# Kernel tuning notes

Hardware: AMD Instinct MI355X
Metric: run time of the kernel (lower is better)

Reference implementation:

```python
import jax, jax.numpy as jnp
import numpy as np

T, B, D, H, O = 512, 256, 512, 256, 256
MLP_DIMS = [(D, 100), (100, 100), (100, 100), (100, 50), (50, H)]


def _linear_init(key, fan_in, fan_out):
    kw, kb = jax.random.split(key)
    lim = 1.0 / np.sqrt(fan_in)
    w = jax.random.uniform(kw, (fan_out, fan_in), minval=-lim, maxval=lim, dtype=jnp.float32)
    b = jax.random.uniform(kb, (fan_out,), minval=-lim, maxval=lim, dtype=jnp.float32)
    return w, b


def setup_inputs() -> dict:
    key = jax.random.key(0)
    ks = jax.random.split(key, 8)
    inp = {"x": jax.random.normal(ks[0], (T, B, D), dtype=jnp.float32)}
    for i, (fi, fo) in enumerate(MLP_DIMS):
        w, b = _linear_init(ks[1 + i], fi, fo)
        inp[f"wm{i + 1}"] = w
        inp[f"bm{i + 1}"] = b
    inp["wx"], inp["bx"] = _linear_init(ks[6], D, H)
    inp["wo"], inp["bo"] = _linear_init(ks[7], H, O)
    return inp


def reference(x, wm1, bm1, wm2, bm2, wm3, bm3, wm4, bm4, wm5, bm5, wx, bx, wo, bo):
    def step(h, xt):
        # xt: [B, D], h: [B, H]
        lx = xt @ wx.T + bx                      # linearX
        a = jax.nn.relu(xt @ wm1.T + bm1)        # layerMLP chain
        a = jax.nn.relu(a @ wm2.T + bm2)
        a = jax.nn.relu(a @ wm3.T + bm3)
        a = jax.nn.relu(a @ wm4.T + bm4)
        fx = jax.nn.sigmoid(a @ wm5.T + bm5)
        gate = fx * jax.nn.sigmoid(lx)
        h_new = jax.nn.relu(jnp.roll(h, 1, axis=-1) + gate)
        return h_new, None

    h0 = jnp.zeros((x.shape[1], wx.shape[0]), dtype=x.dtype)
    hidden, _ = jax.lax.scan(step, h0, x)
    output = hidden @ wo.T + bo                  # h2o
    return output, hidden
```

## Files before the change

kernel.cpp:

```cpp
#include <hip/hip_runtime.h>

typedef __attribute__((ext_vector_type(8))) short short8;
typedef __attribute__((ext_vector_type(4))) float f32x4;

#define OFF_WX 0
#define OFF_W1 131072
#define OFF_W2 188416
#define OFF_W3 202752
#define OFF_W4 217088
#define OFF_W5 225280
#define W_TOTAL 241664

#define TR 32

static __device__ __forceinline__ unsigned short f2bf(float f) {
    unsigned int u = __builtin_bit_cast(unsigned int, f);
    unsigned int r = (u + 0x7fffu + ((u >> 16) & 1u)) >> 16;
    return (unsigned short)r;
}
static __device__ __forceinline__ float bf2f(unsigned short h) {
    unsigned int u = ((unsigned int)h) << 16;
    return __builtin_bit_cast(float, u);
}
static __device__ __forceinline__ float sigmoidf(float z) {
    return 1.f / (1.f + __expf(-z));
}

__global__ __launch_bounds__(256) void prep_kernel(
    const float* __restrict__ wx, const float* __restrict__ wm1,
    const float* __restrict__ wm2, const float* __restrict__ wm3,
    const float* __restrict__ wm4, const float* __restrict__ wm5,
    unsigned short* __restrict__ wb, float* __restrict__ hid)
{
    const int stride = gridDim.x * blockDim.x;
    for (int idx = blockIdx.x * blockDim.x + threadIdx.x; idx < W_TOTAL; idx += stride) {
        float v;
        if (idx < OFF_W1) {
            v = wx[idx];
        } else if (idx < OFF_W2) {
            int j = idx - OFF_W1; int n = j >> 9, k = j & 511;
            v = (n < 100) ? wm1[n * 512 + k] : 0.f;
        } else if (idx < OFF_W3) {
            int j = idx - OFF_W2; int n = j >> 7, k = j & 127;
            v = (n < 100 && k < 100) ? wm2[n * 100 + k] : 0.f;
        } else if (idx < OFF_W4) {
            int j = idx - OFF_W3; int n = j >> 7, k = j & 127;
            v = (n < 100 && k < 100) ? wm3[n * 100 + k] : 0.f;
        } else if (idx < OFF_W5) {
            int j = idx - OFF_W4; int n = j >> 7, k = j & 127;
            v = (n < 50 && k < 100) ? wm4[n * 100 + k] : 0.f;
        } else {
            int j = idx - OFF_W5; int n = j >> 6, k = j & 63;
            v = (k < 50) ? wm5[n * 50 + k] : 0.f;
        }
        wb[idx] = f2bf(v);
    }
    for (int idx = blockIdx.x * blockDim.x + threadIdx.x; idx < 65536; idx += stride)
        hid[idx] = 0.f;
}

template<int KPAD, int NT, int APITCH, int MT, typename Epi>
static __device__ __forceinline__ void stage(const unsigned short* As,
                                             const unsigned short* __restrict__ Wg,
                                             int wave, int lane, Epi&& epi)
{
    constexpr int NI = (NT + 3) >> 2;
    f32x4 acc[NI][MT];
#pragma unroll
    for (int i = 0; i < NI; i++)
#pragma unroll
        for (int mt = 0; mt < MT; mt++)
            acc[i][mt] = {0.f, 0.f, 0.f, 0.f};

    const int kp  = (lane >> 4) << 3;
    const int l15 = lane & 15;

#pragma unroll 4
    for (int k0 = 0; k0 < KPAD; k0 += 32) {
        short8 af[MT];
#pragma unroll
        for (int mt = 0; mt < MT; mt++)
            af[mt] = *(const short8*)(As + (mt * 16 + l15) * APITCH + k0 + kp);
#pragma unroll
        for (int i = 0; i < NI; i++) {
            const int nt = wave + (i << 2);
            if (nt < NT) {
                short8 bf = *(const short8*)(Wg + (nt * 16 + l15) * KPAD + k0 + kp);
#pragma unroll
                for (int mt = 0; mt < MT; mt++)
                    acc[i][mt] = __builtin_amdgcn_mfma_f32_16x16x32_bf16(
                        af[mt], bf, acc[i][mt], 0, 0, 0);
            }
        }
    }
#pragma unroll
    for (int i = 0; i < NI; i++) {
        const int nt = wave + (i << 2);
        if (nt < NT) {
#pragma unroll
            for (int mt = 0; mt < MT; mt++)
                epi(i, nt, mt, acc[i][mt]);
        }
    }
}

__global__ __launch_bounds__(256, 3) void srnn_main(
    const float* __restrict__ x,
    const float* __restrict__ b1, const float* __restrict__ b2,
    const float* __restrict__ b3, const float* __restrict__ b4,
    const float* __restrict__ b5, const float* __restrict__ bx,
    const unsigned short* __restrict__ wb, float* __restrict__ hid)
{
    __shared__ __align__(16) unsigned short Xs[TR * 520];
    __shared__ __align__(16) unsigned short ABuf[2 * TR * 136];
    unsigned short* A1 = ABuf;
    unsigned short* A2 = ABuf + TR * 136;
    unsigned short* Gs = ABuf;

    const int tid  = threadIdx.x;
    const int wave = tid >> 6, lane = tid & 63;
    const int blk  = blockIdx.x;
    const int b    = blk >> 4;
    const int t0   = (blk & 15) << 5;
    const int l15  = lane & 15;
    const int rbase = (lane >> 4) << 2;

    for (int f = tid; f < TR * 128; f += 256) {
        int m = f >> 7, c4 = f & 127;
        const float4* src = (const float4*)(x + ((size_t)(t0 + m) * 256 + b) * 512);
        float4 v = src[c4];
        unsigned int p0 = (unsigned int)f2bf(v.x) | ((unsigned int)f2bf(v.y) << 16);
        unsigned int p1 = (unsigned int)f2bf(v.z) | ((unsigned int)f2bf(v.w) << 16);
        *(uint2*)&Xs[m * 520 + (c4 << 2)] = make_uint2(p0, p1);
    }
    for (int i = tid; i < (2 * TR * 136) / 4; i += 256)
        ((uint2*)ABuf)[i] = make_uint2(0u, 0u);
    __syncthreads();

    stage<512, 7, 520, 2>(Xs, wb + OFF_W1, wave, lane, [&](int, int nt, int mt, f32x4 v) {
        int c = nt * 16 + l15, r = mt * 16 + rbase;
        float bb = (c < 100) ? b1[c] : 0.f;
#pragma unroll
        for (int q = 0; q < 4; q++) {
            float val = (c < 100) ? fmaxf(v[q] + bb, 0.f) : 0.f;
            A1[(r + q) * 136 + c] = f2bf(val);
        }
    });
    __syncthreads();

    stage<128, 7, 136, 2>(A1, wb + OFF_W2, wave, lane, [&](int, int nt, int mt, f32x4 v) {
        int c = nt * 16 + l15, r = mt * 16 + rbase;
        float bb = (c < 100) ? b2[c] : 0.f;
#pragma unroll
        for (int q = 0; q < 4; q++) {
            float val = (c < 100) ? fmaxf(v[q] + bb, 0.f) : 0.f;
            A2[(r + q) * 136 + c] = f2bf(val);
        }
    });
    __syncthreads();

    stage<128, 7, 136, 2>(A2, wb + OFF_W3, wave, lane, [&](int, int nt, int mt, f32x4 v) {
        int c = nt * 16 + l15, r = mt * 16 + rbase;
        float bb = (c < 100) ? b3[c] : 0.f;
#pragma unroll
        for (int q = 0; q < 4; q++) {
            float val = (c < 100) ? fmaxf(v[q] + bb, 0.f) : 0.f;
            A1[(r + q) * 136 + c] = f2bf(val);
        }
    });
    __syncthreads();

    stage<128, 4, 136, 2>(A1, wb + OFF_W4, wave, lane, [&](int, int nt, int mt, f32x4 v) {
        int c = nt * 16 + l15, r = mt * 16 + rbase;
        float bb = (c < 50) ? b4[c] : 0.f;
#pragma unroll
        for (int q = 0; q < 4; q++) {
            float val = (c < 50) ? fmaxf(v[q] + bb, 0.f) : 0.f;
            A2[(r + q) * 136 + c] = f2bf(val);
        }
    });
    __syncthreads();

    f32x4 fxv[4][2];
    stage<64, 16, 136, 2>(A2, wb + OFF_W5, wave, lane, [&](int i, int nt, int mt, f32x4 v) {
        float bb = b5[nt * 16 + l15];
#pragma unroll
        for (int q = 0; q < 4; q++)
            fxv[i][mt][q] = sigmoidf(v[q] + bb);
    });
    __syncthreads();

    stage<512, 16, 520, 2>(Xs, wb + OFF_WX, wave, lane, [&](int i, int nt, int mt, f32x4 v) {
        int c = nt * 16 + l15, r = mt * 16 + rbase;
        float bb = bx[c];
#pragma unroll
        for (int q = 0; q < 4; q++) {
            float g = sigmoidf(v[q] + bb) * fxv[i][mt][q];
            Gs[(r + q) * 264 + c] = f2bf(g);
        }
    });
    __syncthreads();

    {
        const int j = tid;
        const int base = (j + t0 + 1) & 255;
        float ph = 0.f;
#pragma unroll 8
        for (int m = 0; m < TR; m++)
            ph += bf2f(Gs[m * 264 + ((base + m) & 255)]);
        atomicAdd(hid + b * 256 + j, ph);
    }
}

__global__ __launch_bounds__(256) void out_kernel(
    const float* __restrict__ hid, const float* __restrict__ wo,
    const float* __restrict__ bo, float* __restrict__ out)
{
    __shared__ __align__(16) float hrow[256];
    const int b = blockIdx.x, o = threadIdx.x;
    float h = hid[b * 256 + o];
    hrow[o] = h;
    out[65536 + b * 256 + o] = h;
    __syncthreads();
    const float4* wrow = (const float4*)(wo + o * 256);
    float s = bo[o];
#pragma unroll 8
    for (int k4 = 0; k4 < 64; k4++) {
        float4 w = wrow[k4];
        float4 hh = *(const float4*)&hrow[k4 * 4];
        s += hh.x * w.x + hh.y * w.y + hh.z * w.z + hh.w * w.w;
    }
    out[b * 256 + o] = s;
}

extern "C" void kernel_launch(void* const* d_in, const int* in_sizes, int n_in,
                              void* d_out, int out_size, void* d_ws, size_t ws_size,
                              hipStream_t stream)
{
    (void)in_sizes; (void)n_in; (void)out_size; (void)ws_size;
    const float* x   = (const float*)d_in[0];
    const float* wm1 = (const float*)d_in[1];
    const float* bm1 = (const float*)d_in[2];
    const float* wm2 = (const float*)d_in[3];
    const float* bm2 = (const float*)d_in[4];
    const float* wm3 = (const float*)d_in[5];
    const float* bm3 = (const float*)d_in[6];
    const float* wm4 = (const float*)d_in[7];
    const float* bm4 = (const float*)d_in[8];
    const float* wm5 = (const float*)d_in[9];
    const float* bm5 = (const float*)d_in[10];
    const float* wx  = (const float*)d_in[11];
    const float* bx  = (const float*)d_in[12];
    const float* wo  = (const float*)d_in[13];
    const float* bo  = (const float*)d_in[14];
    float* out = (float*)d_out;

    unsigned short* wb = (unsigned short*)d_ws;
    float* hid = (float*)((char*)d_ws + (size_t)W_TOTAL * 2);

    prep_kernel<<<512, 256, 0, stream>>>(wx, wm1, wm2, wm3, wm4, wm5, wb, hid);
    srnn_main<<<4096, 256, 0, stream>>>(x, bm1, bm2, bm3, bm4, bm5, bx, wb, hid);
    out_kernel<<<256, 256, 0, stream>>>(hid, wo, bo, out);
}
```

Baseline: 640.4 us.

## Fuse W1 and Wx GEMMs, swizzle LDS layouts, raise occupancy

The first MLP layer and the linearX projection now run in one K-loop that shares the same X fragment loads, instead of two separate passes over Xs. Padded LDS row pitches are replaced by XOR-swizzled 128/512-element rows, and buffers are aliased to shrink shared memory. This allows raising launch bounds to 4 blocks per CU. The x tile load is also restructured to issue 16 float4 loads per thread before converting, and the ABuf zero-fill is dropped. Fusing keeps more accumulators live, which raises register pressure at the higher occupancy target.

```diff
diff --git a/kernel.cpp b/kernel.cpp
--- a/kernel.cpp
+++ b/kernel.cpp
@@ -5,12 +5,11 @@
 
 #define OFF_WX 0
 #define OFF_W1 131072
-#define OFF_W2 188416
-#define OFF_W3 202752
-#define OFF_W4 217088
-#define OFF_W5 225280
-#define W_TOTAL 241664
-
+#define OFF_W2 196608
+#define OFF_W3 212992
+#define OFF_W4 229376
+#define OFF_W5 237568
+#define W_TOTAL 253952
 #define TR 32
 
 static __device__ __forceinline__ unsigned short f2bf(float f) {
@@ -24,6 +23,9 @@
 }
 static __device__ __forceinline__ float sigmoidf(float z) {
     return 1.f / (1.f + __expf(-z));
+}
+static __device__ __forceinline__ void stA(unsigned short* dst, int r, int c, float v) {
+    dst[(r << 7) + (((c >> 3) ^ (r & 7)) << 3) + (c & 7)] = f2bf(v);
 }
 
 __global__ __launch_bounds__(256) void prep_kernel(
@@ -59,63 +61,53 @@
         hid[idx] = 0.f;
 }
 
-template<int KPAD, int NT, int APITCH, int MT, typename Epi>
-static __device__ __forceinline__ void stage(const unsigned short* As,
-                                             const unsigned short* __restrict__ Wg,
-                                             int wave, int lane, Epi&& epi)
-{
-    constexpr int NI = (NT + 3) >> 2;
-    f32x4 acc[NI][MT];
-#pragma unroll
-    for (int i = 0; i < NI; i++)
-#pragma unroll
-        for (int mt = 0; mt < MT; mt++)
-            acc[i][mt] = {0.f, 0.f, 0.f, 0.f};
-
+template<int KLOOP, int NI, typename Epi>
+static __device__ __forceinline__ void stageS(const unsigned short* As,
+                                              const unsigned short* __restrict__ Wg,
+                                              int wave, int lane, Epi&& epi)
+{
+    f32x4 acc[NI][2];
+#pragma unroll
+    for (int i = 0; i < NI; i++) { acc[i][0] = {0,0,0,0}; acc[i][1] = {0,0,0,0}; }
     const int kp  = (lane >> 4) << 3;
     const int l15 = lane & 15;
-
-#pragma unroll 4
-    for (int k0 = 0; k0 < KPAD; k0 += 32) {
-        short8 af[MT];
-#pragma unroll
-        for (int mt = 0; mt < MT; mt++)
-            af[mt] = *(const short8*)(As + (mt * 16 + l15) * APITCH + k0 + kp);
+#pragma unroll
+    for (int k0 = 0; k0 < KLOOP; k0 += 32) {
+        const int kb = (k0 >> 3) + (lane >> 4);
+        short8 af[2];
+#pragma unroll
+        for (int mt = 0; mt < 2; mt++) {
+            const int rm = mt * 16 + l15;
+            af[mt] = *(const short8*)(As + (rm << 7) + ((kb ^ (rm & 7)) << 3));
+        }
 #pragma unroll
         for (int i = 0; i < NI; i++) {
             const int nt = wave + (i << 2);
-            if (nt < NT) {
-                short8 bf = *(const short8*)(Wg + (nt * 16 + l15) * KPAD + k0 + kp);
-#pragma unroll
-                for (int mt = 0; mt < MT; mt++)
-                    acc[i][mt] = __builtin_amdgcn_mfma_f32_16x16x32_bf16(
-                        af[mt], bf, acc[i][mt], 0, 0, 0);
-            }
-        }
-    }
-#pragma unroll
-    for (int i = 0; i < NI; i++) {
-        const int nt = wave + (i << 2);
-        if (nt < NT) {
-#pragma unroll
-            for (int mt = 0; mt < MT; mt++)
-                epi(i, nt, mt, acc[i][mt]);
-        }
-    }
-}
-
-__global__ __launch_bounds__(256, 3) void srnn_main(
+            short8 bf = *(const short8*)(Wg + (nt * 16 + l15) * KLOOP + k0 + kp);
+#pragma unroll
+            for (int mt = 0; mt < 2; mt++)
+                acc[i][mt] = __builtin_amdgcn_mfma_f32_16x16x32_bf16(
+                    af[mt], bf, acc[i][mt], 0, 0, 0);
+        }
+    }
+#pragma unroll
+    for (int i = 0; i < NI; i++)
+#pragma unroll
+        for (int mt = 0; mt < 2; mt++)
+            epi(i, wave + (i << 2), mt, acc[i][mt]);
+}
+
+__global__ __launch_bounds__(256, 4) void srnn_main(
     const float* __restrict__ x,
     const float* __restrict__ b1, const float* __restrict__ b2,
     const float* __restrict__ b3, const float* __restrict__ b4,
     const float* __restrict__ b5, const float* __restrict__ bx,
     const unsigned short* __restrict__ wb, float* __restrict__ hid)
 {
-    __shared__ __align__(16) unsigned short Xs[TR * 520];
-    __shared__ __align__(16) unsigned short ABuf[2 * TR * 136];
-    unsigned short* A1 = ABuf;
-    unsigned short* A2 = ABuf + TR * 136;
-    unsigned short* Gs = ABuf;
+    __shared__ __align__(16) unsigned short Xs[TR * 512];
+    __shared__ __align__(16) unsigned short A1[TR * 128];
+    unsigned short* A2 = Xs;
+    unsigned short* Gs = Xs + 4096;
 
     const int tid  = threadIdx.x;
     const int wave = tid >> 6, lane = tid & 63;
@@ -123,80 +115,105 @@
     const int b    = blk >> 4;
     const int t0   = (blk & 15) << 5;
     const int l15  = lane & 15;
-    const int rbase = (lane >> 4) << 2;
-
-    for (int f = tid; f < TR * 128; f += 256) {
-        int m = f >> 7, c4 = f & 127;
-        const float4* src = (const float4*)(x + ((size_t)(t0 + m) * 256 + b) * 512);
-        float4 v = src[c4];
-        unsigned int p0 = (unsigned int)f2bf(v.x) | ((unsigned int)f2bf(v.y) << 16);
-        unsigned int p1 = (unsigned int)f2bf(v.z) | ((unsigned int)f2bf(v.w) << 16);
-        *(uint2*)&Xs[m * 520 + (c4 << 2)] = make_uint2(p0, p1);
-    }
-    for (int i = tid; i < (2 * TR * 136) / 4; i += 256)
-        ((uint2*)ABuf)[i] = make_uint2(0u, 0u);
-    __syncthreads();
-
-    stage<512, 7, 520, 2>(Xs, wb + OFF_W1, wave, lane, [&](int, int nt, int mt, f32x4 v) {
-        int c = nt * 16 + l15, r = mt * 16 + rbase;
-        float bb = (c < 100) ? b1[c] : 0.f;
+    const int rb   = (lane >> 4) << 2;
+    const int kp   = (lane >> 4) << 3;
+
+    {
+        const int m0 = tid >> 7, c4 = tid & 127;
+        const float* xbase = x + ((size_t)(t0 + m0) * 256 + b) * 512 + (c4 << 2);
+        float4 xr[16];
+#pragma unroll
+        for (int it = 0; it < 16; it++)
+            xr[it] = *(const float4*)(xbase + (size_t)it * 262144);
+        const int blk8 = c4 >> 1, halfoff = (c4 & 1) << 2;
+#pragma unroll
+        for (int it = 0; it < 16; it++) {
+            const int m = m0 + 2 * it;
+            unsigned int p0 = (unsigned int)f2bf(xr[it].x) | ((unsigned int)f2bf(xr[it].y) << 16);
+            unsigned int p1 = (unsigned int)f2bf(xr[it].z) | ((unsigned int)f2bf(xr[it].w) << 16);
+            *(uint2*)&Xs[(m << 9) + ((blk8 ^ (m & 7)) << 3) + halfoff] = make_uint2(p0, p1);
+        }
+    }
+    __syncthreads();
+
+    f32x4 am1[2][2], alx[4][2];
+#pragma unroll
+    for (int i = 0; i < 2; i++) { am1[i][0] = {0,0,0,0}; am1[i][1] = {0,0,0,0}; }
+#pragma unroll
+    for (int i = 0; i < 4; i++) { alx[i][0] = {0,0,0,0}; alx[i][1] = {0,0,0,0}; }
+    {
+        const unsigned short* W1 = wb + OFF_W1;
+        const unsigned short* WX = wb + OFF_WX;
+#pragma unroll 4
+        for (int k0 = 0; k0 < 512; k0 += 32) {
+            const int kb = (k0 >> 3) + (lane >> 4);
+            short8 af[2];
+#pragma unroll
+            for (int mt = 0; mt < 2; mt++) {
+                const int rm = mt * 16 + l15;
+                af[mt] = *(const short8*)(Xs + (rm << 9) + ((kb ^ (rm & 7)) << 3));
+            }
+#pragma unroll
+            for (int i = 0; i < 2; i++) {
+                short8 bf = *(const short8*)(W1 + ((wave + (i << 2)) * 16 + l15) * 512 + k0 + kp);
+                am1[i][0] = __builtin_amdgcn_mfma_f32_16x16x32_bf16(af[0], bf, am1[i][0], 0, 0, 0);
+                am1[i][1] = __builtin_amdgcn_mfma_f32_16x16x32_bf16(af[1], bf, am1[i][1], 0, 0, 0);
+            }
+#pragma unroll
+            for (int i = 0; i < 4; i++) {
+                short8 bf = *(const short8*)(WX + ((wave + (i << 2)) * 16 + l15) * 512 + k0 + kp);
+                alx[i][0] = __builtin_amdgcn_mfma_f32_16x16x32_bf16(af[0], bf, alx[i][0], 0, 0, 0);
+                alx[i][1] = __builtin_amdgcn_mfma_f32_16x16x32_bf16(af[1], bf, alx[i][1], 0, 0, 0);
+            }
+        }
+#pragma unroll
+        for (int i = 0; i < 2; i++) {
+            const int c = (wave + (i << 2)) * 16 + l15;
+            const float bb = (c < 100) ? b1[c] : 0.f;
+#pragma unroll
+            for (int mt = 0; mt < 2; mt++)
+#pragma unroll
+                for (int q = 0; q < 4; q++)
+                    stA(A1, mt * 16 + rb + q, c,
+                        (c < 100) ? fmaxf(am1[i][mt][q] + bb, 0.f) : 0.f);
+        }
+    }
+    __syncthreads();
+
+    stageS<128, 2>(A1, wb + OFF_W2, wave, lane, [&](int, int nt, int mt, f32x4 v) {
+        const int c = nt * 16 + l15;
+        const float bb = (c < 100) ? b2[c] : 0.f;
+#pragma unroll
+        for (int q = 0; q < 4; q++)
+            stA(A2, mt * 16 + rb + q, c, (c < 100) ? fmaxf(v[q] + bb, 0.f) : 0.f);
+    });
+    __syncthreads();
+
+    stageS<128, 2>(A2, wb + OFF_W3, wave, lane, [&](int, int nt, int mt, f32x4 v) {
+        const int c = nt * 16 + l15;
+        const float bb = (c < 100) ? b3[c] : 0.f;
+#pragma unroll
+        for (int q = 0; q < 4; q++)
+            stA(A1, mt * 16 + rb + q, c, (c < 100) ? fmaxf(v[q] + bb, 0.f) : 0.f);
+    });
+    __syncthreads();
+
+    stageS<128, 1>(A1, wb + OFF_W4, wave, lane, [&](int, int nt, int mt, f32x4 v) {
+        const int c = nt * 16 + l15;
+        const float bb = (c < 50) ? b4[c] : 0.f;
+#pragma unroll
+        for (int q = 0; q < 4; q++)
+            stA(A2, mt * 16 + rb + q, c, (c < 50) ? fmaxf(v[q] + bb, 0.f) : 0.f);
+    });
+    __syncthreads();
+
+    stageS<64, 4>(A2, wb + OFF_W5, wave, lane, [&](int i, int nt, int mt, f32x4 v) {
+        const int c = nt * 16 + l15;
+        const float bb5 = b5[c], bbx = bx[c];
 #pragma unroll
         for (int q = 0; q < 4; q++) {
-            float val = (c < 100) ? fmaxf(v[q] + bb, 0.f) : 0.f;
-            A1[(r + q) * 136 + c] = f2bf(val);
-        }
-    });
-    __syncthreads();
-
-    stage<128, 7, 136, 2>(A1, wb + OFF_W2, wave, lane, [&](int, int nt, int mt, f32x4 v) {
-        int c = nt * 16 + l15, r = mt * 16 + rbase;
-        float bb = (c < 100) ? b2[c] : 0.f;
-#pragma unroll
-        for (int q = 0; q < 4; q++) {
-            float val = (c < 100) ? fmaxf(v[q] + bb, 0.f) : 0.f;
-            A2[(r + q) * 136 + c] = f2bf(val);
-        }
-    });
-    __syncthreads();
-
-    stage<128, 7, 136, 2>(A2, wb + OFF_W3, wave, lane, [&](int, int nt, int mt, f32x4 v) {
-        int c = nt * 16 + l15, r = mt * 16 + rbase;
-        float bb = (c < 100) ? b3[c] : 0.f;
-#pragma unroll
-        for (int q = 0; q < 4; q++) {
-            float val = (c < 100) ? fmaxf(v[q] + bb, 0.f) : 0.f;
-            A1[(r + q) * 136 + c] = f2bf(val);
-        }
-    });
-    __syncthreads();
-
-    stage<128, 4, 136, 2>(A1, wb + OFF_W4, wave, lane, [&](int, int nt, int mt, f32x4 v) {
-        int c = nt * 16 + l15, r = mt * 16 + rbase;
-        float bb = (c < 50) ? b4[c] : 0.f;
-#pragma unroll
-        for (int q = 0; q < 4; q++) {
-            float val = (c < 50) ? fmaxf(v[q] + bb, 0.f) : 0.f;
-            A2[(r + q) * 136 + c] = f2bf(val);
-        }
-    });
-    __syncthreads();
-
-    f32x4 fxv[4][2];
-    stage<64, 16, 136, 2>(A2, wb + OFF_W5, wave, lane, [&](int i, int nt, int mt, f32x4 v) {
-        float bb = b5[nt * 16 + l15];
-#pragma unroll
-        for (int q = 0; q < 4; q++)
-            fxv[i][mt][q] = sigmoidf(v[q] + bb);
-    });
-    __syncthreads();
-
-    stage<512, 16, 520, 2>(Xs, wb + OFF_WX, wave, lane, [&](int i, int nt, int mt, f32x4 v) {
-        int c = nt * 16 + l15, r = mt * 16 + rbase;
-        float bb = bx[c];
-#pragma unroll
-        for (int q = 0; q < 4; q++) {
-            float g = sigmoidf(v[q] + bb) * fxv[i][mt][q];
-            Gs[(r + q) * 264 + c] = f2bf(g);
+            const float g = sigmoidf(v[q] + bb5) * sigmoidf(alx[i][mt][q] + bbx);
+            Gs[(mt * 16 + rb + q) * 256 + c] = f2bf(g);
         }
     });
     __syncthreads();
@@ -205,9 +222,9 @@
         const int j = tid;
         const int base = (j + t0 + 1) & 255;
         float ph = 0.f;
-#pragma unroll 8
+#pragma unroll
         for (int m = 0; m < TR; m++)
-            ph += bf2f(Gs[m * 264 + ((base + m) & 255)]);
+            ph += bf2f(Gs[(m << 8) + ((base + m) & 255)]);
         atomicAdd(hid + b * 256 + j, ph);
     }
 }
```

Result: faster. 610.3 us (-4.7%).
